# Optimization experiments

Hardware: AMD Instinct MI355X
Metric: run time of the kernel (lower is better)

The kernel has to match this reference:

```python
import jax, jax.numpy as jnp
import numpy as np

B, IN_DIM, H, L, P = 256, 64, 768, 4, 8
EPS = 1e-5


def _layernorm(h, g, b):
    mu = jnp.mean(h, axis=-1, keepdims=True)
    var = jnp.mean((h - mu) ** 2, axis=-1, keepdims=True)
    return (h - mu) * jax.lax.rsqrt(var + EPS) * g + b


def setup_inputs() -> dict:
    key = jax.random.key(0)
    ks = jax.random.split(key, 20)
    s_in = 1.0 / np.sqrt(IN_DIM)
    s_h = 1.0 / np.sqrt(H)
    return {
        "x": jax.random.normal(ks[0], (B, IN_DIM), jnp.float32),
        "w_in": jax.random.normal(ks[1], (IN_DIM, H), jnp.float32) * s_in,
        "b_in": jnp.zeros((H,), jnp.float32),
        "ln_g": jnp.ones((L, H), jnp.float32),
        "ln_b": jnp.zeros((L, H), jnp.float32),
        "trop_w": jax.random.normal(ks[2], (L, H, H), jnp.float32) * s_h,  # [L, out, in]
        "trop_b": jnp.zeros((L, H), jnp.float32),
        "lf_amax": jax.random.normal(ks[3], (L, H, P), jnp.float32) * 0.5 + 1.0,
        "lf_bmax": jax.random.normal(ks[4], (L, H, P), jnp.float32) * 0.1,
        "lf_amin": jax.random.normal(ks[5], (L, H, P), jnp.float32) * 0.5 + 1.0,
        "lf_bmin": jax.random.normal(ks[6], (L, H, P), jnp.float32) * 0.1,
        "lf_alpha": jnp.zeros((L, H), jnp.float32),
        "gate_w": jax.random.normal(ks[7], (L, H, H), jnp.float32) * 0.02,
        "gate_b": jnp.full((L, H), 2.0, jnp.float32),
        "cls_w": jax.random.normal(ks[8], (L, H, H), jnp.float32) * s_h,
        "cls_b": jnp.zeros((L, H), jnp.float32),
        "out_g": jnp.ones((H,), jnp.float32),
        "out_b": jnp.zeros((H,), jnp.float32),
        "head_w": jax.random.normal(ks[9], (H, 1), jnp.float32) * s_h,
        "head_b": jnp.zeros((1,), jnp.float32),
    }


def reference(x, w_in, b_in, ln_g, ln_b, trop_w, trop_b, lf_amax, lf_bmax,
              lf_amin, lf_bmin, lf_alpha, gate_w, gate_b, cls_w, cls_b,
              out_g, out_b, head_w, head_b):
    h = x @ w_in + b_in  # [B, H]
    for l in range(L):
        res = h
        hn = _layernorm(h, ln_g[l], ln_b[l])
        # Tropical (max-plus) linear: y[b,o] = max_i(hn[b,i] + W[o,i]) + bias[o]
        t = jnp.max(hn[:, None, :] + trop_w[l][None, :, :], axis=-1) + trop_b[l]
        # LF dual activation: blend of convex (max-plus) and concave (min-plus) PWL
        fmax = jnp.max(t[..., None] * lf_amax[l] + lf_bmax[l], axis=-1)  # [B, H]
        fmin = jnp.min(t[..., None] * lf_amin[l] + lf_bmin[l], axis=-1)
        a = jax.nn.sigmoid(lf_alpha[l])
        trop_out = a * fmax + (1.0 - a) * fmin
        class_out = jax.nn.gelu(hn @ cls_w[l] + cls_b[l], approximate=False)
        g = jax.nn.sigmoid(hn @ gate_w[l] + gate_b[l])
        h = res + g * trop_out + (1.0 - g) * class_out
    h = _layernorm(h, out_g, out_b)
    return (h @ head_w + head_b).squeeze(-1)  # [B]
```

## Files before the change

kernel.cpp:

```cpp
#include <hip/hip_runtime.h>
#include <math.h>

#define HDIM 768
#define BDIM 256
#define INDIM 64
#define NLAYERS 4
#define PDIM 8
#define KSPLIT 24
#define KLEN 32
#define CHK 16
#define TR 128
#define TC 64
#define NTROPBLK 576
#define NCGBLK 192
#define NBLK (NTROPBLK + NCGBLK)

typedef short bf16x8 __attribute__((ext_vector_type(8)));
typedef float f32x4 __attribute__((ext_vector_type(4)));

__device__ __forceinline__ float sigmoidf_(float x) { return 1.f / (1.f + expf(-x)); }
__device__ __forceinline__ float geluf_(float x) { return 0.5f * x * (1.f + erff(x * 0.70710678118654752f)); }
__device__ __forceinline__ unsigned short f2bf(float f) {
    unsigned int u = __float_as_uint(f);
    u += 0x7FFFu + ((u >> 16) & 1u);
    return (unsigned short)(u >> 16);
}

__device__ __forceinline__ void gload_lds16(const float* g, float* l) {
    __builtin_amdgcn_global_load_lds((const __attribute__((address_space(1))) void*)g,
                                     (__attribute__((address_space(3))) void*)l, 16, 0, 0);
}

__global__ __launch_bounds__(256) void prep_k(const float* __restrict__ trop_w,
                                              const float* __restrict__ cls_w,
                                              const float* __restrict__ gate_w,
                                              float* __restrict__ twT,
                                              unsigned short* __restrict__ wB)
{
    __shared__ float tile[64][65];
    const int z = blockIdx.z;
    const int a0 = blockIdx.x * 64;
    const int b0 = blockIdx.y * 64;
    const int c = threadIdx.x & 63;
    const int r4 = threadIdx.x >> 6;

    if (z < NLAYERS) {
        const float* s = trop_w + (size_t)z * HDIM * HDIM;
        float* d = twT + (size_t)z * HDIM * HDIM;
#pragma unroll
        for (int it = 0; it < 16; ++it) {
            const int r = it * 4 + r4;
            tile[r][c] = s[(size_t)(a0 + r) * HDIM + b0 + c];
        }
        __syncthreads();
#pragma unroll
        for (int it = 0; it < 16; ++it) {
            const int r = it * 4 + r4;
            d[(size_t)(b0 + r) * HDIM + a0 + c] = tile[c][r];
        }
    } else {
        const int zz = z - NLAYERS;
        const int l = zz >> 1, mat = zz & 1;
        const float* s = (mat ? gate_w : cls_w) + (size_t)l * HDIM * HDIM;
        unsigned short* d = wB + (size_t)zz * HDIM * HDIM;
#pragma unroll
        for (int it = 0; it < 16; ++it) {
            const int r = it * 4 + r4;
            tile[r][c] = s[(size_t)(b0 + r) * HDIM + a0 + c];
        }
        __syncthreads();
#pragma unroll
        for (int it = 0; it < 16; ++it) {
            const int r = it * 4 + r4;
            d[(size_t)(a0 + r) * HDIM + b0 + c] = f2bf(tile[c][r]);
        }
    }
}

__global__ __launch_bounds__(256) void input_ln_k(
    const float* __restrict__ x, const float* __restrict__ w_in,
    const float* __restrict__ b_in,
    const float* __restrict__ lng, const float* __restrict__ lnb,
    float* __restrict__ h, float* __restrict__ hnT, unsigned short* __restrict__ hnB)
{
    const int b = blockIdx.x;
    const int t = threadIdx.x;
    __shared__ float xs[INDIM];
    __shared__ float rbuf[8];
    if (t < INDIM) xs[t] = x[b * INDIM + t];
    __syncthreads();

    float acc0 = b_in[t], acc1 = b_in[t + 256], acc2 = b_in[t + 512];
#pragma unroll 8
    for (int i = 0; i < INDIM; ++i) {
        const float xv = xs[i];
        acc0 = fmaf(xv, w_in[i * HDIM + t], acc0);
        acc1 = fmaf(xv, w_in[i * HDIM + t + 256], acc1);
        acc2 = fmaf(xv, w_in[i * HDIM + t + 512], acc2);
    }
    h[(size_t)b * HDIM + t] = acc0;
    h[(size_t)b * HDIM + t + 256] = acc1;
    h[(size_t)b * HDIM + t + 512] = acc2;

    float s = acc0 + acc1 + acc2;
    float q = acc0 * acc0 + acc1 * acc1 + acc2 * acc2;
#pragma unroll
    for (int off = 32; off > 0; off >>= 1) { s += __shfl_down(s, off); q += __shfl_down(q, off); }
    const int wid = t >> 6, lane = t & 63;
    if (lane == 0) { rbuf[wid] = s; rbuf[4 + wid] = q; }
    __syncthreads();
    s = rbuf[0] + rbuf[1] + rbuf[2] + rbuf[3];
    q = rbuf[4] + rbuf[5] + rbuf[6] + rbuf[7];
    const float mu = s * (1.f / HDIM);
    const float var = q * (1.f / HDIM) - mu * mu;
    const float rsig = rsqrtf(var + 1e-5f);

#pragma unroll
    for (int qq = 0; qq < 3; ++qq) {
        const int o = t + qq * 256;
        const float av = (qq == 0) ? acc0 : (qq == 1) ? acc1 : acc2;
        const float v = (av - mu) * rsig * lng[o] + lnb[o];
        hnT[(size_t)o * BDIM + b] = v;
        hnB[(size_t)b * HDIM + o] = f2bf(v);
    }
}

__global__ __launch_bounds__(256, 2) void layer_mm_k(
    const float* __restrict__ hnT,
    const float* __restrict__ twT,
    const unsigned short* __restrict__ hnB,
    const unsigned short* __restrict__ wB,
    float* __restrict__ p_trop, float* __restrict__ p_cls, float* __restrict__ p_gate)
{
    __shared__ float hn_s[2][CHK][TR];
    __shared__ float wt_s[2][CHK][TC];

    const int bx = blockIdx.x;
    const int tid = threadIdx.x;
    const int wave = tid >> 6, lane = tid & 63;

    if (bx < NTROPBLK) {
        const int sp = bx % 24;
        const int slot = bx / 24;
        const int col0 = (sp % 12) * TC;
        const int row0 = (sp / 12) * TR;
        const int k0 = slot * KLEN;

        const int tx = tid & 15, ty = tid >> 4;
        const int r0 = ty * 8, c0 = tx * 4;

        const int hk = lane >> 5;
        const int hcol = (lane & 31) * 4;
        const int wr = lane >> 4;
        const int wcol = (lane & 15) * 4;

        float t_acc[8][4];
#pragma unroll
        for (int i = 0; i < 8; ++i)
#pragma unroll
            for (int j = 0; j < 4; ++j) t_acc[i][j] = -1e30f;

        #define STAGE_T(buf, kb)                                                                   \
        {                                                                                          \
            gload_lds16(hnT + (size_t)((kb) + 4 * wave + hk) * BDIM + row0 + hcol,                 \
                        &hn_s[buf][4 * wave][0]);                                                  \
            gload_lds16(hnT + (size_t)((kb) + 4 * wave + 2 + hk) * BDIM + row0 + hcol,             \
                        &hn_s[buf][4 * wave + 2][0]);                                              \
            gload_lds16(twT + (size_t)((kb) + 4 * wave + wr) * HDIM + col0 + wcol,                 \
                        &wt_s[buf][4 * wave][0]);                                                  \
        }

        STAGE_T(0, k0);
        __builtin_amdgcn_s_waitcnt(0);
        __syncthreads();

        for (int c = 0; c < KLEN / CHK; ++c) {
            const int buf = c & 1;
            if (c + 1 < KLEN / CHK) STAGE_T(1 - buf, k0 + (c + 1) * CHK);
#pragma unroll
            for (int k = 0; k < CHK; ++k) {
                const float4 h0 = *(const float4*)&hn_s[buf][k][r0];
                const float4 h1 = *(const float4*)&hn_s[buf][k][r0 + 4];
                const float4 wt = *(const float4*)&wt_s[buf][k][c0];
                const float hf[8] = {h0.x, h0.y, h0.z, h0.w, h1.x, h1.y, h1.z, h1.w};
                const float wtf[4] = {wt.x, wt.y, wt.z, wt.w};
#pragma unroll
                for (int i = 0; i < 8; ++i)
#pragma unroll
                    for (int j = 0; j < 4; ++j)
                        t_acc[i][j] = fmaxf(t_acc[i][j], hf[i] + wtf[j]);
            }
            __builtin_amdgcn_s_waitcnt(0);
            __syncthreads();
        }
        #undef STAGE_T

        const size_t base = (size_t)slot * BDIM * HDIM;
#pragma unroll
        for (int i = 0; i < 8; ++i) {
            const size_t off = base + (size_t)(row0 + r0 + i) * HDIM + col0 + c0;
            *(float4*)(p_trop + off) = make_float4(t_acc[i][0], t_acc[i][1], t_acc[i][2], t_acc[i][3]);
        }
    } else {
        const int cb = bx - NTROPBLK;
        const int mat = cb & 1;
        const int nt = (cb >> 1) % 24;
        const int mt = cb / 48;
        const int m0 = mt * 64 + wave * 16;
        const int n0 = nt * 32;
        const int lm = lane & 15, q = lane >> 4;

        const unsigned short* wmat = wB + (size_t)mat * HDIM * HDIM;
        float* pout = mat ? p_gate : p_cls;

        f32x4 acc[2];
        acc[0] = (f32x4){0.f, 0.f, 0.f, 0.f};
        acc[1] = (f32x4){0.f, 0.f, 0.f, 0.f};

        const unsigned short* aptr = hnB + (size_t)(m0 + lm) * HDIM + q * 8;
        const unsigned short* b0 = wmat + (size_t)(n0 + lm) * HDIM + q * 8;
        const unsigned short* b1 = b0 + (size_t)16 * HDIM;

#pragma unroll 4
        for (int k0 = 0; k0 < HDIM; k0 += 32) {
            const bf16x8 a  = *(const bf16x8*)(aptr + k0);
            const bf16x8 v0 = *(const bf16x8*)(b0 + k0);
            const bf16x8 v1 = *(const bf16x8*)(b1 + k0);
            acc[0] = __builtin_amdgcn_mfma_f32_16x16x32_bf16(a, v0, acc[0], 0, 0, 0);
            acc[1] = __builtin_amdgcn_mfma_f32_16x16x32_bf16(a, v1, acc[1], 0, 0, 0);
        }

#pragma unroll
        for (int nn = 0; nn < 2; ++nn)
#pragma unroll
            for (int r = 0; r < 4; ++r)
                pout[(size_t)(m0 + q * 4 + r) * HDIM + n0 + nn * 16 + lm] = acc[nn][r];
    }
}

__global__ __launch_bounds__(768) void combine_k(
    const float* __restrict__ p_trop, const float* __restrict__ p_cls, const float* __restrict__ p_gate,
    const float* __restrict__ trop_b,
    const float* __restrict__ amax, const float* __restrict__ bmax,
    const float* __restrict__ amin, const float* __restrict__ bmin,
    const float* __restrict__ alpha,
    const float* __restrict__ gate_b, const float* __restrict__ cls_b,
    float* __restrict__ h,
    const float* __restrict__ lng, const float* __restrict__ lnb,
    float* __restrict__ hnT, unsigned short* __restrict__ hnB,
    const float* __restrict__ head_w, const float* __restrict__ head_b,
    float* __restrict__ out, const int is_last)
{
    const int b = blockIdx.x;
    const int o = threadIdx.x;
    __shared__ float rbuf[12], qbuf[12];

    const size_t base = (size_t)b * HDIM + o;
    float tm = -1e30f;
#pragma unroll
    for (int k = 0; k < KSPLIT; ++k)
        tm = fmaxf(tm, p_trop[(size_t)k * BDIM * HDIM + base]);
    const float cs = p_cls[base];
    const float gs = p_gate[base];

    const float tv = tm + trop_b[o];
    float fmx = -1e30f, fmn = 1e30f;
#pragma unroll
    for (int p = 0; p < PDIM; ++p) {
        fmx = fmaxf(fmx, fmaf(tv, amax[o * PDIM + p], bmax[o * PDIM + p]));
        fmn = fminf(fmn, fmaf(tv, amin[o * PDIM + p], bmin[o * PDIM + p]));
    }
    const float a = sigmoidf_(alpha[o]);
    const float trop_out = a * fmx + (1.f - a) * fmn;
    const float cls_out = geluf_(cs + cls_b[o]);
    const float g = sigmoidf_(gs + gate_b[o]);
    const float val = h[base] + g * trop_out + (1.f - g) * cls_out;
    h[base] = val;

    float s = val, q = val * val;
#pragma unroll
    for (int off = 32; off > 0; off >>= 1) { s += __shfl_down(s, off); q += __shfl_down(q, off); }
    const int wid = o >> 6, lane = o & 63;
    if (lane == 0) { rbuf[wid] = s; qbuf[wid] = q; }
    __syncthreads();
    s = 0.f; q = 0.f;
#pragma unroll
    for (int w = 0; w < 12; ++w) { s += rbuf[w]; q += qbuf[w]; }
    const float mu = s * (1.f / HDIM);
    const float var = q * (1.f / HDIM) - mu * mu;
    const float rsig = rsqrtf(var + 1e-5f);
    const float ln_v = (val - mu) * rsig * lng[o] + lnb[o];

    if (!is_last) {
        hnT[(size_t)o * BDIM + b] = ln_v;
        hnB[base] = f2bf(ln_v);
    } else {
        float part = ln_v * head_w[o];
#pragma unroll
        for (int off = 32; off > 0; off >>= 1) part += __shfl_down(part, off);
        __syncthreads();
        if (lane == 0) rbuf[wid] = part;
        __syncthreads();
        if (o == 0) {
            float r = head_b[0];
#pragma unroll
            for (int w = 0; w < 12; ++w) r += rbuf[w];
            out[b] = r;
        }
    }
}

extern "C" void kernel_launch(void* const* d_in, const int* in_sizes, int n_in,
                              void* d_out, int out_size, void* d_ws, size_t ws_size,
                              hipStream_t stream)
{
    const float* x       = (const float*)d_in[0];
    const float* w_in    = (const float*)d_in[1];
    const float* b_in    = (const float*)d_in[2];
    const float* ln_g    = (const float*)d_in[3];
    const float* ln_b    = (const float*)d_in[4];
    const float* trop_w  = (const float*)d_in[5];
    const float* trop_b  = (const float*)d_in[6];
    const float* lf_amax = (const float*)d_in[7];
    const float* lf_bmax = (const float*)d_in[8];
    const float* lf_amin = (const float*)d_in[9];
    const float* lf_bmin = (const float*)d_in[10];
    const float* lf_alpha= (const float*)d_in[11];
    const float* gate_w  = (const float*)d_in[12];
    const float* gate_b  = (const float*)d_in[13];
    const float* cls_w   = (const float*)d_in[14];
    const float* cls_b   = (const float*)d_in[15];
    const float* out_g   = (const float*)d_in[16];
    const float* out_b   = (const float*)d_in[17];
    const float* head_w  = (const float*)d_in[18];
    const float* head_b  = (const float*)d_in[19];
    float* out = (float*)d_out;

    const size_t NBH = (size_t)BDIM * HDIM;
    const size_t WSZ = (size_t)HDIM * HDIM;
    float* ws = (float*)d_ws;
    float* h      = ws;
    float* hnT    = ws + NBH;
    float* twT    = ws + 2 * NBH;
    float* p_trop = twT + (size_t)NLAYERS * WSZ;
    float* p_cls  = p_trop + (size_t)KSPLIT * NBH;
    float* p_gate = p_cls + NBH;
    unsigned short* hnB = (unsigned short*)(p_gate + NBH);
    unsigned short* wB  = hnB + NBH;

    prep_k<<<dim3(12, 12, 12), 256, 0, stream>>>(trop_w, cls_w, gate_w, twT, wB);
    input_ln_k<<<BDIM, 256, 0, stream>>>(x, w_in, b_in, ln_g, ln_b, h, hnT, hnB);

    for (int l = 0; l < NLAYERS; ++l) {
        layer_mm_k<<<NBLK, 256, 0, stream>>>(
            hnT, twT + (size_t)l * WSZ,
            hnB, wB + (size_t)(2 * l) * WSZ,
            p_trop, p_cls, p_gate);

        const int is_last = (l == NLAYERS - 1);
        combine_k<<<BDIM, 768, 0, stream>>>(
            p_trop, p_cls, p_gate,
            trop_b + (size_t)l * HDIM,
            lf_amax + (size_t)l * HDIM * PDIM, lf_bmax + (size_t)l * HDIM * PDIM,
            lf_amin + (size_t)l * HDIM * PDIM, lf_bmin + (size_t)l * HDIM * PDIM,
            lf_alpha + (size_t)l * HDIM,
            gate_b + (size_t)l * HDIM, cls_b + (size_t)l * HDIM,
            h,
            is_last ? out_g : ln_g + (size_t)(l + 1) * HDIM,
            is_last ? out_b : ln_b + (size_t)(l + 1) * HDIM,
            hnT, hnB, head_w, head_b, out, is_last);
    }
}
```

Before: 217.0 us.

## Fuse all stages into one persistent kernel with grid-wide barriers

Replaces the prep, input, per-layer matmul and combine launches with a single persistent kernel of 256 blocks. Stages are separated by atomic-counter grid barriers, which removes the launch overhead of about ten kernel boundaries. The tropical split-K changes from 24 to 16 slices and the MFMA tiling is regrouped so each wave computes three 16-column tiles. The risks are lower parallelism (fewer blocks, with two 256-thread sub-blocks packed per 512-thread block), barrier spin cost, and the assumption that all 256 blocks are co-resident for the barriers to work.

```diff
diff --git a/kernel.cpp b/kernel.cpp
--- a/kernel.cpp
+++ b/kernel.cpp
@@ -6,14 +6,15 @@
 #define INDIM 64
 #define NLAYERS 4
 #define PDIM 8
-#define KSPLIT 24
-#define KLEN 32
+#define KSPLIT 16
+#define KLEN 48
 #define CHK 16
 #define TR 128
 #define TC 64
-#define NTROPBLK 576
-#define NCGBLK 192
-#define NBLK (NTROPBLK + NCGBLK)
+#define NBLKP 256
+#define NTHR 512
+#define WSZ ((size_t)HDIM * HDIM)
+#define NBH ((size_t)BDIM * HDIM)
 
 typedef short bf16x8 __attribute__((ext_vector_type(8)));
 typedef float f32x4 __attribute__((ext_vector_type(4)));
@@ -25,288 +26,308 @@
     u += 0x7FFFu + ((u >> 16) & 1u);
     return (unsigned short)(u >> 16);
 }
-
 __device__ __forceinline__ void gload_lds16(const float* g, float* l) {
     __builtin_amdgcn_global_load_lds((const __attribute__((address_space(1))) void*)g,
                                      (__attribute__((address_space(3))) void*)l, 16, 0, 0);
 }
 
-__global__ __launch_bounds__(256) void prep_k(const float* __restrict__ trop_w,
-                                              const float* __restrict__ cls_w,
-                                              const float* __restrict__ gate_w,
-                                              float* __restrict__ twT,
-                                              unsigned short* __restrict__ wB)
+struct P {
+    const float *x, *w_in, *b_in, *ln_g, *ln_b, *trop_w, *trop_b;
+    const float *amax, *bmax, *amin, *bmin, *alpha;
+    const float *gate_w, *gate_b, *cls_w, *cls_b, *out_g, *out_b, *head_w, *head_b;
+    float *out;
+    float *h, *hnT, *twT, *p_trop, *p_cls, *p_gate;
+    unsigned short *hnB, *wB;
+    int *bar;
+};
+
+union LdsU {
+    struct { float hn[2][CHK][TR]; float wt[2][CHK][TC]; } t[2];
+    float tile[64][65];
+    struct { float xs[2][INDIM]; float rbuf[2][16]; } inp;
+};
+
+__device__ __forceinline__ void gbar(int* cnt, int ph) {
+    __syncthreads();
+    if (threadIdx.x == 0) {
+        __threadfence();
+        __hip_atomic_fetch_add(&cnt[ph], 1, __ATOMIC_RELAXED, __HIP_MEMORY_SCOPE_AGENT);
+        while (__hip_atomic_load(&cnt[ph], __ATOMIC_RELAXED, __HIP_MEMORY_SCOPE_AGENT) < NBLKP)
+            __builtin_amdgcn_s_sleep(8);
+        __threadfence();
+    }
+    __syncthreads();
+}
+
+__global__ __launch_bounds__(NTHR, 2) void mega_k(P p)
 {
-    __shared__ float tile[64][65];
-    const int z = blockIdx.z;
-    const int a0 = blockIdx.x * 64;
-    const int b0 = blockIdx.y * 64;
-    const int c = threadIdx.x & 63;
-    const int r4 = threadIdx.x >> 6;
-
-    if (z < NLAYERS) {
-        const float* s = trop_w + (size_t)z * HDIM * HDIM;
-        float* d = twT + (size_t)z * HDIM * HDIM;
-#pragma unroll
-        for (int it = 0; it < 16; ++it) {
-            const int r = it * 4 + r4;
-            tile[r][c] = s[(size_t)(a0 + r) * HDIM + b0 + c];
-        }
-        __syncthreads();
-#pragma unroll
-        for (int it = 0; it < 16; ++it) {
-            const int r = it * 4 + r4;
-            d[(size_t)(b0 + r) * HDIM + a0 + c] = tile[c][r];
-        }
-    } else {
-        const int zz = z - NLAYERS;
-        const int l = zz >> 1, mat = zz & 1;
-        const float* s = (mat ? gate_w : cls_w) + (size_t)l * HDIM * HDIM;
-        unsigned short* d = wB + (size_t)zz * HDIM * HDIM;
-#pragma unroll
-        for (int it = 0; it < 16; ++it) {
-            const int r = it * 4 + r4;
-            tile[r][c] = s[(size_t)(b0 + r) * HDIM + a0 + c];
-        }
-        __syncthreads();
-#pragma unroll
-        for (int it = 0; it < 16; ++it) {
-            const int r = it * 4 + r4;
-            d[(size_t)(a0 + r) * HDIM + b0 + c] = f2bf(tile[c][r]);
-        }
-    }
-}
-
-__global__ __launch_bounds__(256) void input_ln_k(
-    const float* __restrict__ x, const float* __restrict__ w_in,
-    const float* __restrict__ b_in,
-    const float* __restrict__ lng, const float* __restrict__ lnb,
-    float* __restrict__ h, float* __restrict__ hnT, unsigned short* __restrict__ hnB)
-{
-    const int b = blockIdx.x;
-    const int t = threadIdx.x;
-    __shared__ float xs[INDIM];
-    __shared__ float rbuf[8];
-    if (t < INDIM) xs[t] = x[b * INDIM + t];
-    __syncthreads();
-
-    float acc0 = b_in[t], acc1 = b_in[t + 256], acc2 = b_in[t + 512];
-#pragma unroll 8
-    for (int i = 0; i < INDIM; ++i) {
-        const float xv = xs[i];
-        acc0 = fmaf(xv, w_in[i * HDIM + t], acc0);
-        acc1 = fmaf(xv, w_in[i * HDIM + t + 256], acc1);
-        acc2 = fmaf(xv, w_in[i * HDIM + t + 512], acc2);
-    }
-    h[(size_t)b * HDIM + t] = acc0;
-    h[(size_t)b * HDIM + t + 256] = acc1;
-    h[(size_t)b * HDIM + t + 512] = acc2;
-
-    float s = acc0 + acc1 + acc2;
-    float q = acc0 * acc0 + acc1 * acc1 + acc2 * acc2;
-#pragma unroll
-    for (int off = 32; off > 0; off >>= 1) { s += __shfl_down(s, off); q += __shfl_down(q, off); }
-    const int wid = t >> 6, lane = t & 63;
-    if (lane == 0) { rbuf[wid] = s; rbuf[4 + wid] = q; }
-    __syncthreads();
-    s = rbuf[0] + rbuf[1] + rbuf[2] + rbuf[3];
-    q = rbuf[4] + rbuf[5] + rbuf[6] + rbuf[7];
-    const float mu = s * (1.f / HDIM);
-    const float var = q * (1.f / HDIM) - mu * mu;
-    const float rsig = rsqrtf(var + 1e-5f);
-
-#pragma unroll
-    for (int qq = 0; qq < 3; ++qq) {
-        const int o = t + qq * 256;
-        const float av = (qq == 0) ? acc0 : (qq == 1) ? acc1 : acc2;
-        const float v = (av - mu) * rsig * lng[o] + lnb[o];
-        hnT[(size_t)o * BDIM + b] = v;
-        hnB[(size_t)b * HDIM + o] = f2bf(v);
-    }
-}
-
-__global__ __launch_bounds__(256, 2) void layer_mm_k(
-    const float* __restrict__ hnT,
-    const float* __restrict__ twT,
-    const unsigned short* __restrict__ hnB,
-    const unsigned short* __restrict__ wB,
-    float* __restrict__ p_trop, float* __restrict__ p_cls, float* __restrict__ p_gate)
-{
-    __shared__ float hn_s[2][CHK][TR];
-    __shared__ float wt_s[2][CHK][TC];
-
+    __shared__ LdsU u;
     const int bx = blockIdx.x;
     const int tid = threadIdx.x;
     const int wave = tid >> 6, lane = tid & 63;
-
-    if (bx < NTROPBLK) {
-        const int sp = bx % 24;
-        const int slot = bx / 24;
-        const int col0 = (sp % 12) * TC;
-        const int row0 = (sp / 12) * TR;
-        const int k0 = slot * KLEN;
-
-        const int tx = tid & 15, ty = tid >> 4;
-        const int r0 = ty * 8, c0 = tx * 4;
-
-        const int hk = lane >> 5;
-        const int hcol = (lane & 31) * 4;
-        const int wr = lane >> 4;
-        const int wcol = (lane & 15) * 4;
-
-        float t_acc[8][4];
-#pragma unroll
-        for (int i = 0; i < 8; ++i)
-#pragma unroll
-            for (int j = 0; j < 4; ++j) t_acc[i][j] = -1e30f;
-
-        #define STAGE_T(buf, kb)                                                                   \
-        {                                                                                          \
-            gload_lds16(hnT + (size_t)((kb) + 4 * wave + hk) * BDIM + row0 + hcol,                 \
-                        &hn_s[buf][4 * wave][0]);                                                  \
-            gload_lds16(hnT + (size_t)((kb) + 4 * wave + 2 + hk) * BDIM + row0 + hcol,             \
-                        &hn_s[buf][4 * wave + 2][0]);                                              \
-            gload_lds16(twT + (size_t)((kb) + 4 * wave + wr) * HDIM + col0 + wcol,                 \
-                        &wt_s[buf][4 * wave][0]);                                                  \
-        }
-
-        STAGE_T(0, k0);
-        __builtin_amdgcn_s_waitcnt(0);
+    const int sub = wave >> 2;
+    const int wv = wave & 3;
+    const int stid = tid & 255;
+
+    for (int j = bx; j < 1728; j += NBLKP) {
+        const int c = tid & 63;
+        const int r8 = tid >> 6;
+        if (j < 576) {
+            const int l = j / 144, t = j % 144;
+            const int a0 = (t / 12) * 64, b0 = (t % 12) * 64;
+            const float* s = p.trop_w + (size_t)l * WSZ;
+            float* d = p.twT + (size_t)l * WSZ;
+#pragma unroll
+            for (int it = 0; it < 8; ++it) {
+                const int r = it * 8 + r8;
+                u.tile[r][c] = s[(size_t)(a0 + r) * HDIM + b0 + c];
+            }
+            __syncthreads();
+#pragma unroll
+            for (int it = 0; it < 8; ++it) {
+                const int r = it * 8 + r8;
+                d[(size_t)(b0 + r) * HDIM + a0 + c] = u.tile[c][r];
+            }
+            __syncthreads();
+        } else {
+            const int j2 = j - 576;
+            const int zz = j2 / 144, t = j2 % 144;
+            const int l = zz >> 1, mat = zz & 1;
+            const int a0 = (t / 12) * 64, b0 = (t % 12) * 64;
+            const float* s = (mat ? p.gate_w : p.cls_w) + (size_t)l * WSZ;
+            unsigned short* d = p.wB + (size_t)zz * WSZ;
+#pragma unroll
+            for (int it = 0; it < 8; ++it) {
+                const int r = it * 8 + r8;
+                u.tile[r][c] = s[(size_t)(b0 + r) * HDIM + a0 + c];
+            }
+            __syncthreads();
+#pragma unroll
+            for (int it = 0; it < 8; ++it) {
+                const int r = it * 8 + r8;
+                d[(size_t)(a0 + r) * HDIM + b0 + c] = f2bf(u.tile[c][r]);
+            }
+            __syncthreads();
+        }
+    }
+
+    if (bx < 128) {
+        const int b = bx * 2 + sub;
+        if (stid < INDIM) u.inp.xs[sub][stid] = p.x[b * INDIM + stid];
         __syncthreads();
-
-        for (int c = 0; c < KLEN / CHK; ++c) {
-            const int buf = c & 1;
-            if (c + 1 < KLEN / CHK) STAGE_T(1 - buf, k0 + (c + 1) * CHK);
-#pragma unroll
-            for (int k = 0; k < CHK; ++k) {
-                const float4 h0 = *(const float4*)&hn_s[buf][k][r0];
-                const float4 h1 = *(const float4*)&hn_s[buf][k][r0 + 4];
-                const float4 wt = *(const float4*)&wt_s[buf][k][c0];
-                const float hf[8] = {h0.x, h0.y, h0.z, h0.w, h1.x, h1.y, h1.z, h1.w};
-                const float wtf[4] = {wt.x, wt.y, wt.z, wt.w};
-#pragma unroll
-                for (int i = 0; i < 8; ++i)
-#pragma unroll
-                    for (int j = 0; j < 4; ++j)
-                        t_acc[i][j] = fmaxf(t_acc[i][j], hf[i] + wtf[j]);
-            }
+        float acc0 = p.b_in[stid], acc1 = p.b_in[stid + 256], acc2 = p.b_in[stid + 512];
+#pragma unroll 8
+        for (int i = 0; i < INDIM; ++i) {
+            const float xv = u.inp.xs[sub][i];
+            acc0 = fmaf(xv, p.w_in[i * HDIM + stid], acc0);
+            acc1 = fmaf(xv, p.w_in[i * HDIM + stid + 256], acc1);
+            acc2 = fmaf(xv, p.w_in[i * HDIM + stid + 512], acc2);
+        }
+        p.h[(size_t)b * HDIM + stid] = acc0;
+        p.h[(size_t)b * HDIM + stid + 256] = acc1;
+        p.h[(size_t)b * HDIM + stid + 512] = acc2;
+
+        float s = acc0 + acc1 + acc2;
+        float q = acc0 * acc0 + acc1 * acc1 + acc2 * acc2;
+#pragma unroll
+        for (int off = 32; off > 0; off >>= 1) { s += __shfl_down(s, off); q += __shfl_down(q, off); }
+        if (lane == 0) { u.inp.rbuf[sub][wv] = s; u.inp.rbuf[sub][4 + wv] = q; }
+        __syncthreads();
+        s = u.inp.rbuf[sub][0] + u.inp.rbuf[sub][1] + u.inp.rbuf[sub][2] + u.inp.rbuf[sub][3];
+        q = u.inp.rbuf[sub][4] + u.inp.rbuf[sub][5] + u.inp.rbuf[sub][6] + u.inp.rbuf[sub][7];
+        const float mu = s * (1.f / HDIM);
+        const float var = q * (1.f / HDIM) - mu * mu;
+        const float rsig = rsqrtf(var + 1e-5f);
+#pragma unroll
+        for (int qq = 0; qq < 3; ++qq) {
+            const int o = stid + qq * 256;
+            const float av = (qq == 0) ? acc0 : (qq == 1) ? acc1 : acc2;
+            const float v = (av - mu) * rsig * p.ln_g[o] + p.ln_b[o];
+            p.hnT[(size_t)o * BDIM + b] = v;
+            p.hnB[(size_t)b * HDIM + o] = f2bf(v);
+        }
+    }
+    gbar(p.bar, 0);
+
+    for (int l = 0; l < NLAYERS; ++l) {
+        const float* twTl = p.twT + (size_t)l * WSZ;
+        const unsigned short* wBl = p.wB + (size_t)(2 * l) * WSZ;
+
+        if (bx < 192) {
+            const int s = bx * 2 + sub;
+            const int sp = s % 24;
+            const int slot = s / 24;
+            const int col0 = (sp % 12) * TC;
+            const int row0 = (sp / 12) * TR;
+            const int k0 = slot * KLEN;
+
+            const int tx = stid & 15, ty = stid >> 4;
+            const int r0 = ty * 8, c0 = tx * 4;
+            const int hk = lane >> 5;
+            const int hcol = (lane & 31) * 4;
+            const int wr = lane >> 4;
+            const int wcol = (lane & 15) * 4;
+
+            float t_acc[8][4];
+#pragma unroll
+            for (int i = 0; i < 8; ++i)
+#pragma unroll
+                for (int jj = 0; jj < 4; ++jj) t_acc[i][jj] = -1e30f;
+
+            #define STAGE_T(buf, kb)                                                               \
+            {                                                                                      \
+                gload_lds16(p.hnT + (size_t)((kb) + 4 * wv + hk) * BDIM + row0 + hcol,             \
+                            &u.t[sub].hn[buf][4 * wv][0]);                                         \
+                gload_lds16(p.hnT + (size_t)((kb) + 4 * wv + 2 + hk) * BDIM + row0 + hcol,         \
+                            &u.t[sub].hn[buf][4 * wv + 2][0]);                                     \
+                gload_lds16(twTl + (size_t)((kb) + 4 * wv + wr) * HDIM + col0 + wcol,              \
+                            &u.t[sub].wt[buf][4 * wv][0]);                                         \
+            }
+
+            STAGE_T(0, k0);
             __builtin_amdgcn_s_waitcnt(0);
             __syncthreads();
-        }
-        #undef STAGE_T
-
-        const size_t base = (size_t)slot * BDIM * HDIM;
-#pragma unroll
-        for (int i = 0; i < 8; ++i) {
-            const size_t off = base + (size_t)(row0 + r0 + i) * HDIM + col0 + c0;
-            *(float4*)(p_trop + off) = make_float4(t_acc[i][0], t_acc[i][1], t_acc[i][2], t_acc[i][3]);
-        }
-    } else {
-        const int cb = bx - NTROPBLK;
-        const int mat = cb & 1;
-        const int nt = (cb >> 1) % 24;
-        const int mt = cb / 48;
-        const int m0 = mt * 64 + wave * 16;
-        const int n0 = nt * 32;
-        const int lm = lane & 15, q = lane >> 4;
-
-        const unsigned short* wmat = wB + (size_t)mat * HDIM * HDIM;
-        float* pout = mat ? p_gate : p_cls;
-
-        f32x4 acc[2];
-        acc[0] = (f32x4){0.f, 0.f, 0.f, 0.f};
-        acc[1] = (f32x4){0.f, 0.f, 0.f, 0.f};
-
-        const unsigned short* aptr = hnB + (size_t)(m0 + lm) * HDIM + q * 8;
-        const unsigned short* b0 = wmat + (size_t)(n0 + lm) * HDIM + q * 8;
-        const unsigned short* b1 = b0 + (size_t)16 * HDIM;
+
+            for (int c = 0; c < KLEN / CHK; ++c) {
+                const int buf = c & 1;
+                if (c + 1 < KLEN / CHK) STAGE_T(1 - buf, k0 + (c + 1) * CHK);
+#pragma unroll
+                for (int k = 0; k < CHK; ++k) {
+                    const float4 h0 = *(const float4*)&u.t[sub].hn[buf][k][r0];
+                    const float4 h1 = *(const float4*)&u.t[sub].hn[buf][k][r0 + 4];
+                    const float4 wt = *(const float4*)&u.t[sub].wt[buf][k][c0];
+                    const float hf[8] = {h0.x, h0.y, h0.z, h0.w, h1.x, h1.y, h1.z, h1.w};
+                    const float wtf[4] = {wt.x, wt.y, wt.z, wt.w};
+#pragma unroll
+                    for (int i = 0; i < 8; ++i)
+#pragma unroll
+                        for (int jj = 0; jj < 4; ++jj)
+                            t_acc[i][jj] = fmaxf(t_acc[i][jj], hf[i] + wtf[jj]);
+                }
+                __builtin_amdgcn_s_waitcnt(0);
+                __syncthreads();
+            }
+            #undef STAGE_T
+
+            const size_t base = (size_t)slot * NBH;
+#pragma unroll
+            for (int i = 0; i < 8; ++i) {
+                const size_t off = base + (size_t)(row0 + r0 + i) * HDIM + col0 + c0;
+                *(float4*)(p.p_trop + off) = make_float4(t_acc[i][0], t_acc[i][1], t_acc[i][2], t_acc[i][3]);
+            }
+        } else {
+            const int idx = (bx - 192) * 8 + wave;
+            const int mt = idx >> 5;
+            const int rest = idx & 31;
+            const int mat = rest >> 4;
+            const int nt = rest & 15;
+            const int m0 = mt * 16;
+            const int n0 = nt * 48;
+            const int lm = lane & 15, q = lane >> 4;
+
+            const unsigned short* wmat = wBl + (size_t)mat * WSZ;
+            float* pout = mat ? p.p_gate : p.p_cls;
+
+            f32x4 a0v = (f32x4){0.f, 0.f, 0.f, 0.f};
+            f32x4 a1v = a0v, a2v = a0v;
+
+            const unsigned short* aptr = p.hnB + (size_t)(m0 + lm) * HDIM + q * 8;
+            const unsigned short* b0p = wmat + (size_t)(n0 + lm) * HDIM + q * 8;
+            const unsigned short* b1p = b0p + (size_t)16 * HDIM;
+            const unsigned short* b2p = b0p + (size_t)32 * HDIM;
 
 #pragma unroll 4
-        for (int k0 = 0; k0 < HDIM; k0 += 32) {
-            const bf16x8 a  = *(const bf16x8*)(aptr + k0);
-            const bf16x8 v0 = *(const bf16x8*)(b0 + k0);
-            const bf16x8 v1 = *(const bf16x8*)(b1 + k0);
-            acc[0] = __builtin_amdgcn_mfma_f32_16x16x32_bf16(a, v0, acc[0], 0, 0, 0);
-            acc[1] = __builtin_amdgcn_mfma_f32_16x16x32_bf16(a, v1, acc[1], 0, 0, 0);
-        }
-
-#pragma unroll
-        for (int nn = 0; nn < 2; ++nn)
-#pragma unroll
-            for (int r = 0; r < 4; ++r)
-                pout[(size_t)(m0 + q * 4 + r) * HDIM + n0 + nn * 16 + lm] = acc[nn][r];
-    }
-}
-
-__global__ __launch_bounds__(768) void combine_k(
-    const float* __restrict__ p_trop, const float* __restrict__ p_cls, const float* __restrict__ p_gate,
-    const float* __restrict__ trop_b,
-    const float* __restrict__ amax, const float* __restrict__ bmax,
-    const float* __restrict__ amin, const float* __restrict__ bmin,
-    const float* __restrict__ alpha,
-    const float* __restrict__ gate_b, const float* __restrict__ cls_b,
-    float* __restrict__ h,
-    const float* __restrict__ lng, const float* __restrict__ lnb,
-    float* __restrict__ hnT, unsigned short* __restrict__ hnB,
-    const float* __restrict__ head_w, const float* __restrict__ head_b,
-    float* __restrict__ out, const int is_last)
-{
-    const int b = blockIdx.x;
-    const int o = threadIdx.x;
-    __shared__ float rbuf[12], qbuf[12];
-
-    const size_t base = (size_t)b * HDIM + o;
-    float tm = -1e30f;
-#pragma unroll
-    for (int k = 0; k < KSPLIT; ++k)
-        tm = fmaxf(tm, p_trop[(size_t)k * BDIM * HDIM + base]);
-    const float cs = p_cls[base];
-    const float gs = p_gate[base];
-
-    const float tv = tm + trop_b[o];
-    float fmx = -1e30f, fmn = 1e30f;
-#pragma unroll
-    for (int p = 0; p < PDIM; ++p) {
-        fmx = fmaxf(fmx, fmaf(tv, amax[o * PDIM + p], bmax[o * PDIM + p]));
-        fmn = fminf(fmn, fmaf(tv, amin[o * PDIM + p], bmin[o * PDIM + p]));
-    }
-    const float a = sigmoidf_(alpha[o]);
-    const float trop_out = a * fmx + (1.f - a) * fmn;
-    const float cls_out = geluf_(cs + cls_b[o]);
-    const float g = sigmoidf_(gs + gate_b[o]);
-    const float val = h[base] + g * trop_out + (1.f - g) * cls_out;
-    h[base] = val;
-
-    float s = val, q = val * val;
-#pragma unroll
-    for (int off = 32; off > 0; off >>= 1) { s += __shfl_down(s, off); q += __shfl_down(q, off); }
-    const int wid = o >> 6, lane = o & 63;
-    if (lane == 0) { rbuf[wid] = s; qbuf[wid] = q; }
-    __syncthreads();
-    s = 0.f; q = 0.f;
-#pragma unroll
-    for (int w = 0; w < 12; ++w) { s += rbuf[w]; q += qbuf[w]; }
-    const float mu = s * (1.f / HDIM);
-    const float var = q * (1.f / HDIM) - mu * mu;
-    const float rsig = rsqrtf(var + 1e-5f);
-    const float ln_v = (val - mu) * rsig * lng[o] + lnb[o];
-
-    if (!is_last) {
-        hnT[(size_t)o * BDIM + b] = ln_v;
-        hnB[base] = f2bf(ln_v);
-    } else {
-        float part = ln_v * head_w[o];
-#pragma unroll
-        for (int off = 32; off > 0; off >>= 1) part += __shfl_down(part, off);
-        __syncthreads();
-        if (lane == 0) rbuf[wid] = part;
-        __syncthreads();
-        if (o == 0) {
-            float r = head_b[0];
-#pragma unroll
-            for (int w = 0; w < 12; ++w) r += rbuf[w];
-            out[b] = r;
-        }
+            for (int k0 = 0; k0 < HDIM; k0 += 32) {
+                const bf16x8 a  = *(const bf16x8*)(aptr + k0);
+                const bf16x8 v0 = *(const bf16x8*)(b0p + k0);
+                const bf16x8 v1 = *(const bf16x8*)(b1p + k0);
+                const bf16x8 v2 = *(const bf16x8*)(b2p + k0);
+                a0v = __builtin_amdgcn_mfma_f32_16x16x32_bf16(a, v0, a0v, 0, 0, 0);
+                a1v = __builtin_amdgcn_mfma_f32_16x16x32_bf16(a, v1, a1v, 0, 0, 0);
+                a2v = __builtin_amdgcn_mfma_f32_16x16x32_bf16(a, v2, a2v, 0, 0, 0);
+            }
+#pragma unroll
+            for (int r = 0; r < 4; ++r) {
+                const size_t rowo = (size_t)(m0 + q * 4 + r) * HDIM + n0 + lm;
+                pout[rowo]      = a0v[r];
+                pout[rowo + 16] = a1v[r];
+                pout[rowo + 32] = a2v[r];
+            }
+        }
+        gbar(p.bar, 1 + 2 * l);
+
+        if (bx < 128) {
+            const int b = bx * 2 + sub;
+            const int isl = (l == NLAYERS - 1);
+            const float* lg = isl ? p.out_g : p.ln_g + (size_t)(l + 1) * HDIM;
+            const float* lb = isl ? p.out_b : p.ln_b + (size_t)(l + 1) * HDIM;
+
+            float hv[3];
+            float s = 0.f, q = 0.f;
+#pragma unroll
+            for (int qq = 0; qq < 3; ++qq) {
+                const int o = stid + qq * 256;
+                const size_t base = (size_t)b * HDIM + o;
+                float tm = -1e30f;
+#pragma unroll
+                for (int k = 0; k < KSPLIT; ++k)
+                    tm = fmaxf(tm, p.p_trop[(size_t)k * NBH + base]);
+                const float cs = p.p_cls[base];
+                const float gs = p.p_gate[base];
+
+                const float tv = tm + p.trop_b[l * HDIM + o];
+                float fmx = -1e30f, fmn = 1e30f;
+                const size_t lf = (size_t)l * HDIM * PDIM + (size_t)o * PDIM;
+#pragma unroll
+                for (int pp = 0; pp < PDIM; ++pp) {
+                    fmx = fmaxf(fmx, fmaf(tv, p.amax[lf + pp], p.bmax[lf + pp]));
+                    fmn = fminf(fmn, fmaf(tv, p.amin[lf + pp], p.bmin[lf + pp]));
+                }
+                const float a = sigmoidf_(p.alpha[l * HDIM + o]);
+                const float trop_out = a * fmx + (1.f - a) * fmn;
+                const float cls_out = geluf_(cs + p.cls_b[l * HDIM + o]);
+                const float g = sigmoidf_(gs + p.gate_b[l * HDIM + o]);
+                const float val = p.h[base] + g * trop_out + (1.f - g) * cls_out;
+                hv[qq] = val;
+                p.h[base] = val;
+                s += val; q += val * val;
+            }
+
+#pragma unroll
+            for (int off = 32; off > 0; off >>= 1) { s += __shfl_down(s, off); q += __shfl_down(q, off); }
+            if (lane == 0) { u.inp.rbuf[sub][wv] = s; u.inp.rbuf[sub][4 + wv] = q; }
+            __syncthreads();
+            s = u.inp.rbuf[sub][0] + u.inp.rbuf[sub][1] + u.inp.rbuf[sub][2] + u.inp.rbuf[sub][3];
+            q = u.inp.rbuf[sub][4] + u.inp.rbuf[sub][5] + u.inp.rbuf[sub][6] + u.inp.rbuf[sub][7];
+            const float mu = s * (1.f / HDIM);
+            const float var = q * (1.f / HDIM) - mu * mu;
+            const float rsig = rsqrtf(var + 1e-5f);
+
+            if (!isl) {
+#pragma unroll
+                for (int qq = 0; qq < 3; ++qq) {
+                    const int o = stid + qq * 256;
+                    const float ln_v = (hv[qq] - mu) * rsig * lg[o] + lb[o];
+                    p.hnT[(size_t)o * BDIM + b] = ln_v;
+                    p.hnB[(size_t)b * HDIM + o] = f2bf(ln_v);
+                }
+            } else {
+                float part = 0.f;
+#pragma unroll
+                for (int qq = 0; qq < 3; ++qq) {
+                    const int o = stid + qq * 256;
+                    part += ((hv[qq] - mu) * rsig * lg[o] + lb[o]) * p.head_w[o];
+                }
+#pragma unroll
+                for (int off = 32; off > 0; off >>= 1) part += __shfl_down(part, off);
+                if (lane == 0) u.inp.rbuf[sub][8 + wv] = part;
+                __syncthreads();
+                if (stid == 0)
+                    p.out[b] = u.inp.rbuf[sub][8] + u.inp.rbuf[sub][9]
+                             + u.inp.rbuf[sub][10] + u.inp.rbuf[sub][11] + p.head_b[0];
+            }
+        }
+        if (l < NLAYERS - 1) gbar(p.bar, 2 + 2 * l);
     }
 }
 
@@ -314,60 +335,40 @@
                               void* d_out, int out_size, void* d_ws, size_t ws_size,
                               hipStream_t stream)
 {
-    const float* x       = (const float*)d_in[0];
-    const float* w_in    = (const float*)d_in[1];
-    const float* b_in    = (const float*)d_in[2];
-    const float* ln_g    = (const float*)d_in[3];
-    const float* ln_b    = (const float*)d_in[4];
-    const float* trop_w  = (const float*)d_in[5];
-    const float* trop_b  = (const float*)d_in[6];
-    const float* lf_amax = (const float*)d_in[7];
-    const float* lf_bmax = (const float*)d_in[8];
-    const float* lf_amin = (const float*)d_in[9];
-    const float* lf_bmin = (const float*)d_in[10];
-    const float* lf_alpha= (const float*)d_in[11];
-    const float* gate_w  = (const float*)d_in[12];
-    const float* gate_b  = (const float*)d_in[13];
-    const float* cls_w   = (const float*)d_in[14];
-    const float* cls_b   = (const float*)d_in[15];
-    const float* out_g   = (const float*)d_in[16];
-    const float* out_b   = (const float*)d_in[17];
-    const float* head_w  = (const float*)d_in[18];
-    const float* head_b  = (const float*)d_in[19];
-    float* out = (float*)d_out;
-
-    const size_t NBH = (size_t)BDIM * HDIM;
-    const size_t WSZ = (size_t)HDIM * HDIM;
+    P pp;
+    pp.x      = (const float*)d_in[0];
+    pp.w_in   = (const float*)d_in[1];
+    pp.b_in   = (const float*)d_in[2];
+    pp.ln_g   = (const float*)d_in[3];
+    pp.ln_b   = (const float*)d_in[4];
+    pp.trop_w = (const float*)d_in[5];
+    pp.trop_b = (const float*)d_in[6];
+    pp.amax   = (const float*)d_in[7];
+    pp.bmax   = (const float*)d_in[8];
+    pp.amin   = (const float*)d_in[9];
+    pp.bmin   = (const float*)d_in[10];
+    pp.alpha  = (const float*)d_in[11];
+    pp.gate_w = (const float*)d_in[12];
+    pp.gate_b = (const float*)d_in[13];
+    pp.cls_w  = (const float*)d_in[14];
+    pp.cls_b  = (const float*)d_in[15];
+    pp.out_g  = (const float*)d_in[16];
+    pp.out_b  = (const float*)d_in[17];
+    pp.head_w = (const float*)d_in[18];
+    pp.head_b = (const float*)d_in[19];
+    pp.out    = (float*)d_out;
+
     float* ws = (float*)d_ws;
-    float* h      = ws;
-    float* hnT    = ws + NBH;
-    float* twT    = ws + 2 * NBH;
-    float* p_trop = twT + (size_t)NLAYERS * WSZ;
-    float* p_cls  = p_trop + (size_t)KSPLIT * NBH;
-    float* p_gate = p_cls + NBH;
-    unsigned short* hnB = (unsigned short*)(p_gate + NBH);
-    unsigned short* wB  = hnB + NBH;
-
-    prep_k<<<dim3(12, 12, 12), 256, 0, stream>>>(trop_w, cls_w, gate_w, twT, wB);
-    input_ln_k<<<BDIM, 256, 0, stream>>>(x, w_in, b_in, ln_g, ln_b, h, hnT, hnB);
-
-    for (int l = 0; l < NLAYERS; ++l) {
-        layer_mm_k<<<NBLK, 256, 0, stream>>>(
-            hnT, twT + (size_t)l * WSZ,
-            hnB, wB + (size_t)(2 * l) * WSZ,
-            p_trop, p_cls, p_gate);
-
-        const int is_last = (l == NLAYERS - 1);
-        combine_k<<<BDIM, 768, 0, stream>>>(
-            p_trop, p_cls, p_gate,
-            trop_b + (size_t)l * HDIM,
-            lf_amax + (size_t)l * HDIM * PDIM, lf_bmax + (size_t)l * HDIM * PDIM,
-            lf_amin + (size_t)l * HDIM * PDIM, lf_bmin + (size_t)l * HDIM * PDIM,
-            lf_alpha + (size_t)l * HDIM,
-            gate_b + (size_t)l * HDIM, cls_b + (size_t)l * HDIM,
-            h,
-            is_last ? out_g : ln_g + (size_t)(l + 1) * HDIM,
-            is_last ? out_b : ln_b + (size_t)(l + 1) * HDIM,
-            hnT, hnB, head_w, head_b, out, is_last);
-    }
-}
+    pp.h      = ws;
+    pp.hnT    = ws + NBH;
+    pp.twT    = ws + 2 * NBH;
+    pp.p_trop = pp.twT + (size_t)NLAYERS * WSZ;
+    pp.p_cls  = pp.p_trop + (size_t)KSPLIT * NBH;
+    pp.p_gate = pp.p_cls + NBH;
+    pp.hnB    = (unsigned short*)(pp.p_gate + NBH);
+    pp.wB     = pp.hnB + NBH;
+    pp.bar    = (int*)(pp.wB + 8 * WSZ);
+
+    hipMemsetAsync(pp.bar, 0, 16 * sizeof(int), stream);
+    mega_k<<<NBLKP, NTHR, 0, stream>>>(pp);
+}
```

New measurement: 452.5 us. 109% more time.
